# Optimization experiments

Measured on AMD Instinct MI355X. Metric: run time of the kernel, lower is better.

Reference implementation:

```python
import jax, jax.numpy as jnp
import numpy as np

LOW_A, LOW_B = 32 // 4, 32 // 4  # spatial_shape=(32,32) default -> keep 8x8 low freqs


def _dct_basis(K, N, dtype):
    # Unnormalized DCT-II basis (torch_dct norm=None): C[k,n] = 2*cos(pi*(2n+1)k/(2N))
    n = jnp.arange(N, dtype=jnp.float32)
    k = jnp.arange(K, dtype=jnp.float32)
    return (2.0 * jnp.cos(jnp.pi * (2.0 * n[None, :] + 1.0) * k[:, None] / (2.0 * N))).astype(dtype)


def setup_inputs() -> dict:
    key = jax.random.key(0)
    delta = jax.random.normal(key, (256, 3, 256, 256), dtype=jnp.float32)
    return {"delta": delta}


def reference(delta):
    B, C, H, W = delta.shape
    Ch = _dct_basis(LOW_A, H, delta.dtype)  # [a, H]
    Cw = _dct_basis(LOW_B, W, delta.dtype)  # [b, W]
    # Equivalent to dct_2d(delta)[:, :, :a, :b]: truncated DCT along H then W.
    low = jnp.einsum('ih,nchw,jw->ncij', Ch, delta, Cw)  # [B, C, a, b]
    return jnp.abs(low).mean()
```

## Files before the change

kernel.cpp:

```cpp
#include <hip/hip_runtime.h>


#define INV_COUNT (1.0f / 49152.0f)

__global__ __launch_bounds__(256, 3) void lowfreq_main(
    const float* __restrict__ delta, float* __restrict__ ws,
    float* __restrict__ out)
{
    __shared__ float c_row[256][8];
    __shared__ float c_col[8][256];
    __shared__ float pacc[4][64];

    const int t = threadIdx.x;
    const int wave = t >> 6;
    const int lane = t & 63;
    const int bid = blockIdx.x;
    const int img = bid >> 1;
    const int half = bid & 1;

    {
        const float a = 3.14159265358979323846f * (2.0f * (float)t + 1.0f)
                        * (1.0f / 512.0f);
        const float ca = cosf(a);
        float ckm1 = 1.0f;
        float ck   = ca;
        c_row[t][0] = 2.0f;  c_col[0][t] = 2.0f;
        c_row[t][1] = 2.0f * ca;  c_col[1][t] = 2.0f * ca;
        #pragma unroll
        for (int k = 2; k < 8; ++k) {
            const float cn = 2.0f * ca * ck - ckm1;
            ckm1 = ck; ck = cn;
            c_row[t][k] = 2.0f * cn;
            c_col[k][t] = 2.0f * cn;
        }
    }
    __syncthreads();

    const int row0 = (half << 7) + (wave << 5);
    const float* gp = delta + (size_t)img * 65536 + (size_t)row0 * 256 + lane;

    float u[4][8];
    #pragma unroll
    for (int c = 0; c < 4; ++c)
        #pragma unroll
        for (int i = 0; i < 8; ++i) u[c][i] = 0.0f;

    #pragma unroll 4
    for (int r = 0; r < 32; ++r) {
        const int h = row0 + r;
        const float x0 = gp[r * 256 + 0];
        const float x1 = gp[r * 256 + 64];
        const float x2 = gp[r * 256 + 128];
        const float x3 = gp[r * 256 + 192];
        const float4 cA = *reinterpret_cast<const float4*>(&c_row[h][0]);
        const float4 cB = *reinterpret_cast<const float4*>(&c_row[h][4]);
        const float cc[8] = {cA.x, cA.y, cA.z, cA.w, cB.x, cB.y, cB.z, cB.w};
        #pragma unroll
        for (int i = 0; i < 8; ++i) {
            u[0][i] = fmaf(cc[i], x0, u[0][i]);
            u[1][i] = fmaf(cc[i], x1, u[1][i]);
            u[2][i] = fmaf(cc[i], x2, u[2][i]);
            u[3][i] = fmaf(cc[i], x3, u[3][i]);
        }
    }

    float cw[4][8];
    #pragma unroll
    for (int c = 0; c < 4; ++c)
        #pragma unroll
        for (int j = 0; j < 8; ++j)
            cw[c][j] = c_col[j][(c << 6) + lane];

    float v[64];
    #pragma unroll
    for (int i = 0; i < 8; ++i)
        #pragma unroll
        for (int j = 0; j < 8; ++j) {
            float s = u[0][i] * cw[0][j];
            s = fmaf(u[1][i], cw[1][j], s);
            s = fmaf(u[2][i], cw[2][j], s);
            s = fmaf(u[3][i], cw[3][j], s);
            v[(i << 3) + j] = s;
        }

    #pragma unroll
    for (int s = 0; s < 6; ++s) {
        const int m = 1 << s;
        const bool bit = (lane & m) != 0;
        #pragma unroll
        for (int k = 0; k < (64 >> (s + 1)); ++k) {
            const float a = v[2 * k];
            const float b = v[2 * k + 1];
            const float keep = bit ? b : a;
            const float send = bit ? a : b;
            const float recv = __shfl_xor(send, m, 64);
            v[k] = keep + recv;
        }
    }

    pacc[wave][lane] = v[0];
    __syncthreads();

    if (t < 64) {
        const float s4 = pacc[0][t] + pacc[1][t] + pacc[2][t] + pacc[3][t];
        ws[(size_t)bid * 64 + t] = s4;
        if (bid == 0 && t == 0) out[0] = 0.0f;
    }
}

__global__ __launch_bounds__(256) void lowfreq_reduce(
    const float* __restrict__ ws, float* __restrict__ out)
{
    __shared__ float acc[4];
    const int t = threadIdx.x;
    const int wave = t >> 6;
    const int lane = t & 63;
    const int g = blockIdx.x * 256 + t;
    const int img = g >> 6;
    const int slot = g & 63;

    const float s = ws[(size_t)(2 * img) * 64 + slot]
                  + ws[(size_t)(2 * img + 1) * 64 + slot];
    float a = fabsf(s);
    #pragma unroll
    for (int m = 1; m < 64; m <<= 1) a += __shfl_xor(a, m, 64);
    if (lane == 0) acc[wave] = a;
    __syncthreads();
    if (t == 0)
        atomicAdd(out, (acc[0] + acc[1] + acc[2] + acc[3]) * INV_COUNT);
}

extern "C" void kernel_launch(void* const* d_in, const int* in_sizes, int n_in,
                              void* d_out, int out_size, void* d_ws, size_t ws_size,
                              hipStream_t stream)
{
    const float* delta = (const float*)d_in[0];
    float* out = (float*)d_out;
    float* ws = (float*)d_ws;
    lowfreq_main<<<1536, 256, 0, stream>>>(delta, ws, out);
    lowfreq_reduce<<<192, 256, 0, stream>>>(ws, out);
}
```

Before: 40.48 us.

## Split each image into four row quarters and batch row loads

Each image is now covered by four blocks instead of two, so each wave handles 16 rows and the grid doubles to 3072 blocks. The row loop is fully unrolled in groups of four rows, with all sixteen global loads of a group issued before the FMAs so more memory requests are in flight. The reduce kernel now sums four partials per image. This adds per-block overhead: the DCT table setup, the butterfly shuffle reduction and twice as many partial writes.

```diff
diff --git a/kernel.cpp b/kernel.cpp
--- a/kernel.cpp
+++ b/kernel.cpp
@@ -15,8 +15,8 @@
     const int wave = t >> 6;
     const int lane = t & 63;
     const int bid = blockIdx.x;
-    const int img = bid >> 1;
-    const int half = bid & 1;
+    const int img = bid >> 2;
+    const int q = bid & 3;
 
     {
         const float a = 3.14159265358979323846f * (2.0f * (float)t + 1.0f)
@@ -24,7 +24,7 @@
         const float ca = cosf(a);
         float ckm1 = 1.0f;
         float ck   = ca;
-        c_row[t][0] = 2.0f;  c_col[0][t] = 2.0f;
+        c_row[t][0] = 2.0f;       c_col[0][t] = 2.0f;
         c_row[t][1] = 2.0f * ca;  c_col[1][t] = 2.0f * ca;
         #pragma unroll
         for (int k = 2; k < 8; ++k) {
@@ -36,7 +36,7 @@
     }
     __syncthreads();
 
-    const int row0 = (half << 7) + (wave << 5);
+    const int row0 = (q << 6) + (wave << 4);
     const float* gp = delta + (size_t)img * 65536 + (size_t)row0 * 256 + lane;
 
     float u[4][8];
@@ -45,22 +45,30 @@
         #pragma unroll
         for (int i = 0; i < 8; ++i) u[c][i] = 0.0f;
 
-    #pragma unroll 4
-    for (int r = 0; r < 32; ++r) {
-        const int h = row0 + r;
-        const float x0 = gp[r * 256 + 0];
-        const float x1 = gp[r * 256 + 64];
-        const float x2 = gp[r * 256 + 128];
-        const float x3 = gp[r * 256 + 192];
-        const float4 cA = *reinterpret_cast<const float4*>(&c_row[h][0]);
-        const float4 cB = *reinterpret_cast<const float4*>(&c_row[h][4]);
-        const float cc[8] = {cA.x, cA.y, cA.z, cA.w, cB.x, cB.y, cB.z, cB.w};
+    #pragma unroll
+    for (int rb = 0; rb < 4; ++rb) {
+        float x[4][4];
         #pragma unroll
-        for (int i = 0; i < 8; ++i) {
-            u[0][i] = fmaf(cc[i], x0, u[0][i]);
-            u[1][i] = fmaf(cc[i], x1, u[1][i]);
-            u[2][i] = fmaf(cc[i], x2, u[2][i]);
-            u[3][i] = fmaf(cc[i], x3, u[3][i]);
+        for (int rr = 0; rr < 4; ++rr) {
+            const float* p = gp + (size_t)((rb << 2) + rr) * 256;
+            x[rr][0] = p[0];
+            x[rr][1] = p[64];
+            x[rr][2] = p[128];
+            x[rr][3] = p[192];
+        }
+        #pragma unroll
+        for (int rr = 0; rr < 4; ++rr) {
+            const int h = row0 + (rb << 2) + rr;
+            const float4 cA = *reinterpret_cast<const float4*>(&c_row[h][0]);
+            const float4 cB = *reinterpret_cast<const float4*>(&c_row[h][4]);
+            const float cc[8] = {cA.x, cA.y, cA.z, cA.w, cB.x, cB.y, cB.z, cB.w};
+            #pragma unroll
+            for (int i = 0; i < 8; ++i) {
+                u[0][i] = fmaf(cc[i], x[rr][0], u[0][i]);
+                u[1][i] = fmaf(cc[i], x[rr][1], u[1][i]);
+                u[2][i] = fmaf(cc[i], x[rr][2], u[2][i]);
+                u[3][i] = fmaf(cc[i], x[rr][3], u[3][i]);
+            }
         }
     }
 
@@ -119,8 +127,10 @@
     const int img = g >> 6;
     const int slot = g & 63;
 
-    const float s = ws[(size_t)(2 * img) * 64 + slot]
-                  + ws[(size_t)(2 * img + 1) * 64 + slot];
+    const float s = ws[(size_t)(4 * img + 0) * 64 + slot]
+                  + ws[(size_t)(4 * img + 1) * 64 + slot]
+                  + ws[(size_t)(4 * img + 2) * 64 + slot]
+                  + ws[(size_t)(4 * img + 3) * 64 + slot];
     float a = fabsf(s);
     #pragma unroll
     for (int m = 1; m < 64; m <<= 1) a += __shfl_xor(a, m, 64);
@@ -137,6 +147,6 @@
     const float* delta = (const float*)d_in[0];
     float* out = (float*)d_out;
     float* ws = (float*)d_ws;
-    lowfreq_main<<<1536, 256, 0, stream>>>(delta, ws, out);
+    lowfreq_main<<<3072, 256, 0, stream>>>(delta, ws, out);
     lowfreq_reduce<<<192, 256, 0, stream>>>(ws, out);
 }
```

New measurement: 41.31 us. +2.0%, slower.

## Fuse final reduction into main kernel via last-block atomics and LDS column DCT

Applied to the files above, without the earlier changes.

Replaces the per-lane 64-output column transform and its shuffle butterfly reduction with a staged LDS accumulation of row-transformed data. Each lane then computes one (i,j) coefficient by a dot product over LDS. The separate reduce kernel is removed: paired blocks use an atomic counter to combine halves, and a global done-counter lets the last block write the mean. This also raises the occupancy hint to 4 blocks per CU. It adds a memset launch and serialized __syncthreads stages in exchange for fewer registers and no second kernel.

```diff
diff --git a/kernel.cpp b/kernel.cpp
--- a/kernel.cpp
+++ b/kernel.cpp
@@ -2,13 +2,16 @@
 
 
 #define INV_COUNT (1.0f / 49152.0f)
+#define NBLK 1536
+#define CTRL_OFF (NBLK * 64)
 
-__global__ __launch_bounds__(256, 3) void lowfreq_main(
+__global__ __launch_bounds__(256, 4) void lowfreq_main(
     const float* __restrict__ delta, float* __restrict__ ws,
     float* __restrict__ out)
 {
-    __shared__ float c_row[256][8];
-    __shared__ float c_col[8][256];
+    __shared__ __align__(16) float c_row[256][8];
+    __shared__ __align__(16) float c_col[8][260];
+    __shared__ __align__(16) float u_lds[8][260];
     __shared__ float pacc[4][64];
 
     const int t = threadIdx.x;
@@ -22,9 +25,8 @@
         const float a = 3.14159265358979323846f * (2.0f * (float)t + 1.0f)
                         * (1.0f / 512.0f);
         const float ca = cosf(a);
-        float ckm1 = 1.0f;
-        float ck   = ca;
-        c_row[t][0] = 2.0f;  c_col[0][t] = 2.0f;
+        float ckm1 = 1.0f, ck = ca;
+        c_row[t][0] = 2.0f;       c_col[0][t] = 2.0f;
         c_row[t][1] = 2.0f * ca;  c_col[1][t] = 2.0f * ca;
         #pragma unroll
         for (int k = 2; k < 8; ++k) {
@@ -64,70 +66,65 @@
         }
     }
 
-    float cw[4][8];
     #pragma unroll
-    for (int c = 0; c < 4; ++c)
+    for (int s = 0; s < 4; ++s) {
+        if (wave == s) {
+            #pragma unroll
+            for (int i = 0; i < 8; ++i)
+                #pragma unroll
+                for (int c = 0; c < 4; ++c) {
+                    const int w = (c << 6) + lane;
+                    if (s == 0) u_lds[i][w] = u[c][i];
+                    else        u_lds[i][w] += u[c][i];
+                }
+        }
+        __syncthreads();
+    }
+
+    {
+        const int i = lane >> 3;
+        const int j = lane & 7;
+        const int w0 = wave << 6;
+        float acc = 0.0f;
         #pragma unroll
-        for (int j = 0; j < 8; ++j)
-            cw[c][j] = c_col[j][(c << 6) + lane];
+        for (int k = 0; k < 16; ++k) {
+            const float4 uv = *reinterpret_cast<const float4*>(&u_lds[i][w0 + (k << 2)]);
+            const float4 cv = *reinterpret_cast<const float4*>(&c_col[j][w0 + (k << 2)]);
+            acc = fmaf(uv.x, cv.x, acc);
+            acc = fmaf(uv.y, cv.y, acc);
+            acc = fmaf(uv.z, cv.z, acc);
+            acc = fmaf(uv.w, cv.w, acc);
+        }
+        pacc[wave][lane] = acc;
+    }
+    __syncthreads();
 
-    float v[64];
-    #pragma unroll
-    for (int i = 0; i < 8; ++i)
-        #pragma unroll
-        for (int j = 0; j < 8; ++j) {
-            float s = u[0][i] * cw[0][j];
-            s = fmaf(u[1][i], cw[1][j], s);
-            s = fmaf(u[2][i], cw[2][j], s);
-            s = fmaf(u[3][i], cw[3][j], s);
-            v[(i << 3) + j] = s;
-        }
-
-    #pragma unroll
-    for (int s = 0; s < 6; ++s) {
-        const int m = 1 << s;
-        const bool bit = (lane & m) != 0;
-        #pragma unroll
-        for (int k = 0; k < (64 >> (s + 1)); ++k) {
-            const float a = v[2 * k];
-            const float b = v[2 * k + 1];
-            const float keep = bit ? b : a;
-            const float send = bit ? a : b;
-            const float recv = __shfl_xor(send, m, 64);
-            v[k] = keep + recv;
+    if (wave == 0) {
+        const float s4 = pacc[0][lane] + pacc[1][lane] + pacc[2][lane] + pacc[3][lane];
+        ws[(size_t)bid * 64 + lane] = s4;
+        __threadfence();
+        int arrived = 0;
+        if (lane == 0)
+            arrived = atomicAdd((int*)(ws + CTRL_OFF) + img, 1);
+        arrived = __shfl(arrived, 0, 64);
+        if (arrived == 1) {
+            __threadfence();
+            const float oth = ws[(size_t)(bid ^ 1) * 64 + lane];
+            float a = fabsf(s4 + oth);
+            #pragma unroll
+            for (int m = 1; m < 64; m <<= 1) a += __shfl_xor(a, m, 64);
+            if (lane == 0) {
+                float* accum = ws + CTRL_OFF + 768;
+                int* done = (int*)(ws + CTRL_OFF) + 769;
+                atomicAdd(accum, a);
+                __threadfence();
+                if (atomicAdd(done, 1) == 767) {
+                    __threadfence();
+                    out[0] = atomicAdd(accum, 0.0f) * INV_COUNT;
+                }
+            }
         }
     }
-
-    pacc[wave][lane] = v[0];
-    __syncthreads();
-
-    if (t < 64) {
-        const float s4 = pacc[0][t] + pacc[1][t] + pacc[2][t] + pacc[3][t];
-        ws[(size_t)bid * 64 + t] = s4;
-        if (bid == 0 && t == 0) out[0] = 0.0f;
-    }
-}
-
-__global__ __launch_bounds__(256) void lowfreq_reduce(
-    const float* __restrict__ ws, float* __restrict__ out)
-{
-    __shared__ float acc[4];
-    const int t = threadIdx.x;
-    const int wave = t >> 6;
-    const int lane = t & 63;
-    const int g = blockIdx.x * 256 + t;
-    const int img = g >> 6;
-    const int slot = g & 63;
-
-    const float s = ws[(size_t)(2 * img) * 64 + slot]
-                  + ws[(size_t)(2 * img + 1) * 64 + slot];
-    float a = fabsf(s);
-    #pragma unroll
-    for (int m = 1; m < 64; m <<= 1) a += __shfl_xor(a, m, 64);
-    if (lane == 0) acc[wave] = a;
-    __syncthreads();
-    if (t == 0)
-        atomicAdd(out, (acc[0] + acc[1] + acc[2] + acc[3]) * INV_COUNT);
 }
 
 extern "C" void kernel_launch(void* const* d_in, const int* in_sizes, int n_in,
@@ -137,6 +134,6 @@
     const float* delta = (const float*)d_in[0];
     float* out = (float*)d_out;
     float* ws = (float*)d_ws;
-    lowfreq_main<<<1536, 256, 0, stream>>>(delta, ws, out);
-    lowfreq_reduce<<<192, 256, 0, stream>>>(ws, out);
+    hipMemsetAsync((char*)d_ws + (size_t)CTRL_OFF * 4, 0, 770 * 4, stream);
+    lowfreq_main<<<NBLK, 256, 0, stream>>>(delta, ws, out);
 }
```

Result: slower. 141.5 us (+249.6%).

## Fuse final reduction into main kernel via per-image arrival counters

Applied to the files above, without the earlier changes.

Removes the separate reduce kernel. Each image's second-arriving block combines both halves, applies abs and a wave reduction, and atomically accumulates into a global scalar. A done counter lets the last block write the output. This swaps a kernel launch for a memset launch plus atomics and fences, and the float atomic accumulation order becomes nondeterministic.

```diff
diff --git a/kernel.cpp b/kernel.cpp
--- a/kernel.cpp
+++ b/kernel.cpp
@@ -2,6 +2,8 @@
 
 
 #define INV_COUNT (1.0f / 49152.0f)
+#define NBLK 1536
+#define CTRL_OFF (NBLK * 64)
 
 __global__ __launch_bounds__(256, 3) void lowfreq_main(
     const float* __restrict__ delta, float* __restrict__ ws,
@@ -22,9 +24,8 @@
         const float a = 3.14159265358979323846f * (2.0f * (float)t + 1.0f)
                         * (1.0f / 512.0f);
         const float ca = cosf(a);
-        float ckm1 = 1.0f;
-        float ck   = ca;
-        c_row[t][0] = 2.0f;  c_col[0][t] = 2.0f;
+        float ckm1 = 1.0f, ck = ca;
+        c_row[t][0] = 2.0f;       c_col[0][t] = 2.0f;
         c_row[t][1] = 2.0f * ca;  c_col[1][t] = 2.0f * ca;
         #pragma unroll
         for (int k = 2; k < 8; ++k) {
@@ -101,33 +102,33 @@
     pacc[wave][lane] = v[0];
     __syncthreads();
 
-    if (t < 64) {
-        const float s4 = pacc[0][t] + pacc[1][t] + pacc[2][t] + pacc[3][t];
-        ws[(size_t)bid * 64 + t] = s4;
-        if (bid == 0 && t == 0) out[0] = 0.0f;
+    if (wave == 0) {
+        const float s4 = pacc[0][lane] + pacc[1][lane]
+                       + pacc[2][lane] + pacc[3][lane];
+        ws[(size_t)bid * 64 + lane] = s4;
+        __threadfence();
+        int arrived = 0;
+        if (lane == 0)
+            arrived = atomicAdd((int*)(ws + CTRL_OFF) + img, 1);
+        arrived = __shfl(arrived, 0, 64);
+        if (arrived == 1) {
+            __threadfence();
+            const float oth = ws[(size_t)(bid ^ 1) * 64 + lane];
+            float a = fabsf(s4 + oth);
+            #pragma unroll
+            for (int m = 1; m < 64; m <<= 1) a += __shfl_xor(a, m, 64);
+            if (lane == 0) {
+                float* accum = ws + CTRL_OFF + 768;
+                int* done = (int*)(ws + CTRL_OFF) + 769;
+                atomicAdd(accum, a * INV_COUNT);
+                __threadfence();
+                if (atomicAdd(done, 1) == 767) {
+                    __threadfence();
+                    out[0] = atomicAdd(accum, 0.0f);
+                }
+            }
+        }
     }
-}
-
-__global__ __launch_bounds__(256) void lowfreq_reduce(
-    const float* __restrict__ ws, float* __restrict__ out)
-{
-    __shared__ float acc[4];
-    const int t = threadIdx.x;
-    const int wave = t >> 6;
-    const int lane = t & 63;
-    const int g = blockIdx.x * 256 + t;
-    const int img = g >> 6;
-    const int slot = g & 63;
-
-    const float s = ws[(size_t)(2 * img) * 64 + slot]
-                  + ws[(size_t)(2 * img + 1) * 64 + slot];
-    float a = fabsf(s);
-    #pragma unroll
-    for (int m = 1; m < 64; m <<= 1) a += __shfl_xor(a, m, 64);
-    if (lane == 0) acc[wave] = a;
-    __syncthreads();
-    if (t == 0)
-        atomicAdd(out, (acc[0] + acc[1] + acc[2] + acc[3]) * INV_COUNT);
 }
 
 extern "C" void kernel_launch(void* const* d_in, const int* in_sizes, int n_in,
@@ -137,6 +138,6 @@
     const float* delta = (const float*)d_in[0];
     float* out = (float*)d_out;
     float* ws = (float*)d_ws;
-    lowfreq_main<<<1536, 256, 0, stream>>>(delta, ws, out);
-    lowfreq_reduce<<<192, 256, 0, stream>>>(ws, out);
+    hipMemsetAsync((char*)d_ws + (size_t)CTRL_OFF * 4, 0, 770 * 4, stream);
+    lowfreq_main<<<NBLK, 256, 0, stream>>>(delta, ws, out);
 }
```

Result: slower. 140.5 us (+247.0%).
